# Optimization experiments

Measured on AMD Instinct MI355X. Metric: run time of the kernel, lower is better.

## Reference

```python
import jax, jax.numpy as jnp
import numpy as np

M = 1024       # input feature dim
T_EXPERTS = 64 # number of experts
K = 2          # top-k
TOKENS = 65536 # B*N flattened tokens


def setup_inputs() -> dict:
    key = jax.random.key(0)
    ks = jax.random.split(key, 6)
    return {
        "x": jax.random.normal(ks[0], (TOKENS, M), dtype=jnp.float32),
        "noise": jax.random.normal(ks[1], (TOKENS, T_EXPERTS), dtype=jnp.float32),
        "Wg_w": jax.random.normal(ks[2], (T_EXPERTS, M), dtype=jnp.float32) * 0.02,
        "Wg_b": jax.random.normal(ks[3], (T_EXPERTS,), dtype=jnp.float32) * 0.02,
        "Wn_w": jax.random.normal(ks[4], (T_EXPERTS, M), dtype=jnp.float32) * 0.02,
        "Wn_b": jax.random.normal(ks[5], (T_EXPERTS,), dtype=jnp.float32) * 0.02,
    }


def reference(x, noise, Wg_w, Wg_b, Wn_w, Wn_b):
    # logits = Wg(x); noise_scale = softplus(Wnoise(x))
    logits = jnp.einsum("bm,tm->bt", x, Wg_w) + Wg_b          # [tokens, t]
    noise_scale = jax.nn.softplus(jnp.einsum("bm,tm->bt", x, Wn_w) + Wn_b)
    H = logits + noise * noise_scale                           # noisy logits
    topk_vals, topk_idx = jax.lax.top_k(H, K)                  # [tokens, k]
    topk_softmax = jax.nn.softmax(topk_vals, axis=-1)
    # scatter softmax weights into sparse [tokens, t] gate tensor
    rows = jnp.arange(H.shape[0])[:, None]
    gates = jnp.zeros_like(H).at[rows, topk_idx].set(topk_softmax)
    return (gates, H, topk_idx, noise_scale, logits)
```

## Files before the change

kernel.cpp:

```cpp
#include <hip/hip_runtime.h>
#include <math.h>

#define NTOK 65536
#define MDIM 1024
#define NE   64
#define TB   128
#define NKC  32
#define DELTA 5e-4f

typedef float f32x4  __attribute__((ext_vector_type(4)));
typedef float f32x2  __attribute__((ext_vector_type(2)));
typedef short bf16x8 __attribute__((ext_vector_type(8)));
typedef unsigned int u32;

__device__ __forceinline__ unsigned short f32_to_bf16_rne(float f) {
    u32 u = __builtin_bit_cast(u32, f);
    u32 r = u + 0x7FFFu + ((u >> 16) & 1u);
    return (unsigned short)(r >> 16);
}
__device__ __forceinline__ float bf16_to_f32(unsigned short h) {
    u32 u = ((u32)h) << 16;
    return __builtin_bit_cast(float, u);
}
__device__ __forceinline__ void gll16(const void* g, void* l) {
    __builtin_amdgcn_global_load_lds(
        (const __attribute__((address_space(1))) u32*)g,
        (__attribute__((address_space(3))) u32*)l, 16, 0, 0);
}
__device__ __forceinline__ void nt_store4(float* p, f32x4 v) {
    __builtin_nontemporal_store(v, (f32x4*)p);
}

__global__ __launch_bounds__(256) void split_w_kernel(
    const float* __restrict__ Wg_w, const float* __restrict__ Wn_w,
    unsigned short* __restrict__ ws, u32* __restrict__ cnt)
{
    if (blockIdx.x == 0 && threadIdx.x == 0) *cnt = 0;

    const int gid  = blockIdx.x * 256 + threadIdx.x;
    const int kc   = gid >> 10;
    const int rest = gid & 1023;
    const int tm   = rest >> 8;
    const int mat  = (rest >> 7) & 1;
    const int sp   = (rest >> 6) & 1;
    const int lane = rest & 63;
    const int e    = (lane & 15) + 16 * tm;
    const int k0   = kc * 32 + 8 * (lane >> 4);
    const float* W = mat ? Wn_w : Wg_w;

    unsigned short o[8];
#pragma unroll
    for (int i = 0; i < 8; ++i) {
        const float v = W[(size_t)e * MDIM + k0 + i];
        const u32 u  = __builtin_bit_cast(u32, v);
        const unsigned short hb = (unsigned short)(u >> 16);
        o[i] = sp ? f32_to_bf16_rne(v - bf16_to_f32(hb)) : hb;
    }
    uint4 pk;
    pk.x = (u32)o[0] | ((u32)o[1] << 16);
    pk.y = (u32)o[2] | ((u32)o[3] << 16);
    pk.z = (u32)o[4] | ((u32)o[5] << 16);
    pk.w = (u32)o[6] | ((u32)o[7] << 16);
    *reinterpret_cast<uint4*>(&ws[(size_t)gid * 8]) = pk;
}

__global__ __launch_bounds__(512, 6) void gate_mfma_kernel(
    const float* __restrict__ x,
    const float* __restrict__ noise,
    const unsigned short* __restrict__ ws,
    const float* __restrict__ Wg_b,
    const float* __restrict__ Wn_b,
    float* __restrict__ out_gates,
    float* __restrict__ out_H,
    float* __restrict__ out_idx,
    float* __restrict__ out_ns,
    float* __restrict__ out_logits,
    u32* __restrict__ cnt,
    u32* __restrict__ list)
{
    __shared__ unsigned short wbuf[2][8192];

    const int tid   = threadIdx.x;
    const int lane  = tid & 63;
    const int w     = tid >> 6;
    const int c     = lane & 15;
    const int q     = lane >> 4;
    const int tokw  = blockIdx.x * TB + w * 16;
    const int phase = blockIdx.x & (NKC - 1);

    const float* __restrict__ xr = x + (size_t)(tokw + c) * MDIM + 8 * q;

    f32x4 acc[4][2];
#pragma unroll
    for (int tm = 0; tm < 4; ++tm)
#pragma unroll
        for (int m = 0; m < 2; ++m)
            acc[tm][m] = (f32x4){0.f, 0.f, 0.f, 0.f};

    f32x4 xa, xb;

#define STAGE(CI, BUF)                                                          \
    {                                                                           \
        const unsigned short* wc_ = ws + (size_t)(CI) * 8192;                   \
        gll16(wc_ + (size_t)tid * 8,         &wbuf[BUF][(size_t)tid * 8]);      \
        gll16(wc_ + (size_t)(tid + 512) * 8, &wbuf[BUF][(size_t)(tid + 512) * 8]); \
        __builtin_amdgcn_sched_barrier(0);                                      \
        xa = *reinterpret_cast<const f32x4*>(xr + (CI) * 32);                   \
        xb = *reinterpret_cast<const f32x4*>(xr + (CI) * 32 + 4);               \
        __builtin_amdgcn_sched_barrier(0);                                      \
    }

    STAGE(phase, 0)
    asm volatile("s_waitcnt vmcnt(2)" ::: "memory");
    __syncthreads();

    int cur = 0;
    for (int kci = 0; kci < NKC; ++kci) {
        asm volatile("s_waitcnt vmcnt(0)" ::: "memory");

        bf16x8 xhi, xlo;
        {
            const float v[8] = {xa.x, xa.y, xa.z, xa.w, xb.x, xb.y, xb.z, xb.w};
            u32 hp[4], lp[4];
#pragma unroll
            for (int p = 0; p < 4; ++p) {
                const u32 u0 = __builtin_bit_cast(u32, v[2 * p]);
                const u32 u1 = __builtin_bit_cast(u32, v[2 * p + 1]);
                const float h0 = __builtin_bit_cast(float, u0 & 0xFFFF0000u);
                const float h1 = __builtin_bit_cast(float, u1 & 0xFFFF0000u);
                hp[p] = (u0 >> 16) | (u1 & 0xFFFF0000u);
                const u32 l0 = (u32)f32_to_bf16_rne(v[2 * p] - h0);
                const u32 l1 = (u32)f32_to_bf16_rne(v[2 * p + 1] - h1);
                lp[p] = l0 | (l1 << 16);
            }
            const uint4 h4 = {hp[0], hp[1], hp[2], hp[3]};
            const uint4 l4 = {lp[0], lp[1], lp[2], lp[3]};
            xhi = __builtin_bit_cast(bf16x8, h4);
            xlo = __builtin_bit_cast(bf16x8, l4);
        }

        if (kci + 1 < NKC) {
            const int kcn = (kci + 1 + phase) & (NKC - 1);
            STAGE(kcn, cur ^ 1)
        }

#pragma unroll
        for (int tm = 0; tm < 4; ++tm)
#pragma unroll
            for (int mat = 0; mat < 2; ++mat) {
                const int gbase = ((tm * 4 + mat * 2) * 64 + lane) * 8;
                const bf16x8 whi = *reinterpret_cast<const bf16x8*>(&wbuf[cur][gbase]);
                const bf16x8 wlo = *reinterpret_cast<const bf16x8*>(&wbuf[cur][gbase + 512]);
                f32x4 a = acc[tm][mat];
                a = __builtin_amdgcn_mfma_f32_16x16x32_bf16(wlo, xhi, a, 0, 0, 0);
                a = __builtin_amdgcn_mfma_f32_16x16x32_bf16(whi, xlo, a, 0, 0, 0);
                a = __builtin_amdgcn_mfma_f32_16x16x32_bf16(whi, xhi, a, 0, 0, 0);
                acc[tm][mat] = a;
            }

        if (kci + 1 < NKC) {
            asm volatile("s_waitcnt vmcnt(2)" ::: "memory");
            __syncthreads();
        }
        cur ^= 1;
    }
#undef STAGE

    f32x4 bgv[4], bnv[4];
#pragma unroll
    for (int tm = 0; tm < 4; ++tm) {
        bgv[tm] = *reinterpret_cast<const f32x4*>(&Wg_b[16 * tm + 4 * q]);
        bnv[tm] = *reinterpret_cast<const f32x4*>(&Wn_b[16 * tm + 4 * q]);
    }

    const int tok = tokw + c;
    float hv[4][4];

#pragma unroll
    for (int tm = 0; tm < 4; ++tm) {
        const size_t rb = (size_t)tok * NE + 16 * tm + 4 * q;
        const f32x4 nz = __builtin_nontemporal_load(
            reinterpret_cast<const f32x4*>(&noise[rb]));
        f32x4 lg, nsv, hh;
#pragma unroll
        for (int r = 0; r < 4; ++r) {
            lg[r] = acc[tm][0][r] + bgv[tm][r];
            const float nl = acc[tm][1][r] + bnv[tm][r];
            nsv[r] = fmaxf(nl, 0.f) + log1pf(expf(-fabsf(nl)));
            hh[r]  = fmaf(nz[r], nsv[r], lg[r]);
            hv[tm][r] = hh[r];
        }
        nt_store4(&out_logits[rb], lg);
        nt_store4(&out_ns[rb],     nsv);
        nt_store4(&out_H[rb],      hh);
    }

    float v1 = -INFINITY, v2 = -INFINITY, v3 = -INFINITY;
    int   i1 = 0,         i2 = 0;
#pragma unroll
    for (int tm = 0; tm < 4; ++tm)
#pragma unroll
        for (int r = 0; r < 4; ++r) {
            const int ex = 16 * tm + 4 * q + r;
            const float hcur = hv[tm][r];
            if (hcur > v1)      { v3 = v2; v2 = v1; i2 = i1; v1 = hcur; i1 = ex; }
            else if (hcur > v2) { v3 = v2; v2 = hcur; i2 = ex; }
            else if (hcur > v3) { v3 = hcur; }
        }

#pragma unroll
    for (int off = 16; off <= 32; off <<= 1) {
        const float w1 = __shfl_xor(v1, off, 64);
        const int   k1 = __shfl_xor(i1, off, 64);
        const float w2 = __shfl_xor(v2, off, 64);
        const int   k2 = __shfl_xor(i2, off, 64);
        const float w3 = __shfl_xor(v3, off, 64);
        float m3;
        if (v1 >= w1) m3 = (v2 >= w1) ? fmaxf(v3, w1) : fmaxf(v2, w2);
        else          m3 = (w2 >= v1) ? fmaxf(w3, v1) : fmaxf(w2, v2);
        if (w1 > v1 || (w1 == v1 && k1 < i1)) {
            if (v1 > w2 || (v1 == w2 && i1 < k2)) { v2 = v1; i2 = i1; }
            else                                  { v2 = w2; i2 = k2; }
            v1 = w1; i1 = k1;
        } else {
            if (w1 > v2 || (w1 == v2 && k1 < i2)) { v2 = w1; i2 = k1; }
        }
        v3 = m3;
    }

    const float e2v = expf(v2 - v1);
    const float inv = 1.f / (1.f + e2v);
    const float p1  = inv;
    const float p2  = e2v * inv;

#pragma unroll
    for (int tm = 0; tm < 4; ++tm) {
        f32x4 g;
#pragma unroll
        for (int r = 0; r < 4; ++r) {
            const int ex = 16 * tm + 4 * q + r;
            g[r] = (ex == i1) ? p1 : ((ex == i2) ? p2 : 0.f);
        }
        nt_store4(&out_gates[(size_t)tok * NE + 16 * tm + 4 * q], g);
    }
    if (q == 0) {
        f32x2 iv;
        iv.x = (float)i1;
        iv.y = (float)i2;
        __builtin_nontemporal_store(iv,
            reinterpret_cast<f32x2*>(&out_idx[(size_t)tok * 2]));
        if ((v1 - v2 < DELTA) || (v2 - v3 < DELTA)) {
            const u32 slot = atomicAdd(cnt, 1u);
            list[slot] = (u32)tok;
        }
    }
}

__global__ __launch_bounds__(64) void refine_kernel(
    const float* __restrict__ x,
    const float* __restrict__ noise,
    const float* __restrict__ Wg_w, const float* __restrict__ Wg_b,
    const float* __restrict__ Wn_w, const float* __restrict__ Wn_b,
    const u32* __restrict__ cnt, const u32* __restrict__ list,
    float* __restrict__ out_gates, float* __restrict__ out_idx)
{
    const int lane = threadIdx.x;
    const u32 n = *cnt;

    for (u32 it = blockIdx.x; it < n; it += gridDim.x) {
        const int tok = (int)list[it];

        f32x4 xv[4];
#pragma unroll
        for (int i = 0; i < 4; ++i)
            xv[i] = *reinterpret_cast<const f32x4*>(
                &x[(size_t)tok * MDIM + lane * 16 + i * 4]);

        float lgv = 0.f, nlv = 0.f;
        for (int e = 0; e < NE; ++e) {
            float sg = 0.f, sn = 0.f;
#pragma unroll
            for (int i = 0; i < 4; ++i) {
                const f32x4 wg = *reinterpret_cast<const f32x4*>(
                    &Wg_w[(size_t)e * MDIM + lane * 16 + i * 4]);
                const f32x4 wn = *reinterpret_cast<const f32x4*>(
                    &Wn_w[(size_t)e * MDIM + lane * 16 + i * 4]);
#pragma unroll
                for (int j = 0; j < 4; ++j) {
                    sg = fmaf(xv[i][j], wg[j], sg);
                    sn = fmaf(xv[i][j], wn[j], sn);
                }
            }
#pragma unroll
            for (int off = 32; off >= 1; off >>= 1) {
                sg += __shfl_xor(sg, off, 64);
                sn += __shfl_xor(sn, off, 64);
            }
            if (e == lane) { lgv = sg; nlv = sn; }
        }

        lgv += Wg_b[lane];
        nlv += Wn_b[lane];
        const float ns = fmaxf(nlv, 0.f) + log1pf(expf(-fabsf(nlv)));
        const float h  = fmaf(noise[(size_t)tok * NE + lane], ns, lgv);

        float v1 = h; int i1 = lane;
#pragma unroll
        for (int off = 32; off >= 1; off >>= 1) {
            const float ov = __shfl_xor(v1, off, 64);
            const int   oi = __shfl_xor(i1, off, 64);
            if (ov > v1 || (ov == v1 && oi < i1)) { v1 = ov; i1 = oi; }
        }
        float v2 = (lane == i1) ? -INFINITY : h; int i2 = lane;
#pragma unroll
        for (int off = 32; off >= 1; off >>= 1) {
            const float ov = __shfl_xor(v2, off, 64);
            const int   oi = __shfl_xor(i2, off, 64);
            if (ov > v2 || (ov == v2 && oi < i2)) { v2 = ov; i2 = oi; }
        }

        const float e2v = expf(v2 - v1);
        const float inv = 1.f / (1.f + e2v);
        const float p1  = inv;
        const float p2  = e2v * inv;

        out_gates[(size_t)tok * NE + lane] =
            (lane == i1) ? p1 : ((lane == i2) ? p2 : 0.f);
        if (lane == 0) {
            *reinterpret_cast<float2*>(&out_idx[(size_t)tok * 2]) =
                make_float2((float)i1, (float)i2);
        }
    }
}

extern "C" void kernel_launch(void* const* d_in, const int* in_sizes, int n_in,
                              void* d_out, int out_size, void* d_ws, size_t ws_size,
                              hipStream_t stream) {
    const float* x     = (const float*)d_in[0];
    const float* noise = (const float*)d_in[1];
    const float* Wg_w  = (const float*)d_in[2];
    const float* Wg_b  = (const float*)d_in[3];
    const float* Wn_w  = (const float*)d_in[4];
    const float* Wn_b  = (const float*)d_in[5];

    float* out = (float*)d_out;
    float* out_gates  = out;
    float* out_H      = out + (size_t)NTOK * NE;
    float* out_idx    = out + (size_t)2 * NTOK * NE;
    float* out_ns     = out + (size_t)2 * NTOK * NE + (size_t)NTOK * 2;
    float* out_logits = out + (size_t)3 * NTOK * NE + (size_t)NTOK * 2;

    unsigned short* wsplit = (unsigned short*)d_ws;
    u32* cnt  = (u32*)((char*)d_ws + 524288);
    u32* list = (u32*)((char*)d_ws + 524304);

    split_w_kernel<<<dim3(128), dim3(256), 0, stream>>>(Wg_w, Wn_w, wsplit, cnt);
    gate_mfma_kernel<<<dim3(NTOK / TB), dim3(512), 0, stream>>>(
        x, noise, wsplit, Wg_b, Wn_b,
        out_gates, out_H, out_idx, out_ns, out_logits, cnt, list);
    refine_kernel<<<dim3(1024), dim3(64), 0, stream>>>(
        x, noise, Wg_w, Wg_b, Wn_w, Wn_b, cnt, list, out_gates, out_idx);
}
```

Baseline: 121.0 us.

## Prefetch x fragments two k-chunks ahead with double-buffered registers

The x register loads are split from the weight LDS staging and issued two iterations ahead into a pair of register sets. The top-of-loop full vmcnt(0) wait goes away and the end-of-iteration waits are adjusted, so global x loads have more time in flight. Launch bounds drop from 6 to 5 waves per SIMD so the extra registers fit, which may lower occupancy.

```diff
diff --git a/kernel.cpp b/kernel.cpp
--- a/kernel.cpp
+++ b/kernel.cpp
@@ -64,7 +64,7 @@
     *reinterpret_cast<uint4*>(&ws[(size_t)gid * 8]) = pk;
 }
 
-__global__ __launch_bounds__(512, 6) void gate_mfma_kernel(
+__global__ __launch_bounds__(512, 5) void gate_mfma_kernel(
     const float* __restrict__ x,
     const float* __restrict__ noise,
     const unsigned short* __restrict__ ws,
@@ -97,30 +97,37 @@
         for (int m = 0; m < 2; ++m)
             acc[tm][m] = (f32x4){0.f, 0.f, 0.f, 0.f};
 
-    f32x4 xa, xb;
-
-#define STAGE(CI, BUF)                                                          \
+    f32x4 xa[2], xb[2];
+
+#define WGLL(CI, BUF)                                                           \
     {                                                                           \
         const unsigned short* wc_ = ws + (size_t)(CI) * 8192;                   \
         gll16(wc_ + (size_t)tid * 8,         &wbuf[BUF][(size_t)tid * 8]);      \
         gll16(wc_ + (size_t)(tid + 512) * 8, &wbuf[BUF][(size_t)(tid + 512) * 8]); \
         __builtin_amdgcn_sched_barrier(0);                                      \
-        xa = *reinterpret_cast<const f32x4*>(xr + (CI) * 32);                   \
-        xb = *reinterpret_cast<const f32x4*>(xr + (CI) * 32 + 4);               \
+    }
+#define XLOAD(CI, SET)                                                          \
+    {                                                                           \
+        xa[SET] = *reinterpret_cast<const f32x4*>(xr + (CI) * 32);              \
+        xb[SET] = *reinterpret_cast<const f32x4*>(xr + (CI) * 32 + 4);          \
         __builtin_amdgcn_sched_barrier(0);                                      \
     }
 
-    STAGE(phase, 0)
+    WGLL(phase, 0)
+    XLOAD(phase, 0)
+    XLOAD((phase + 1) & (NKC - 1), 1)
     asm volatile("s_waitcnt vmcnt(2)" ::: "memory");
     __syncthreads();
 
     int cur = 0;
     for (int kci = 0; kci < NKC; ++kci) {
-        asm volatile("s_waitcnt vmcnt(0)" ::: "memory");
+        const int st = kci & 1;
 
         bf16x8 xhi, xlo;
         {
-            const float v[8] = {xa.x, xa.y, xa.z, xa.w, xb.x, xb.y, xb.z, xb.w};
+            const f32x4 a = xa[st];
+            const f32x4 b = xb[st];
+            const float v[8] = {a.x, a.y, a.z, a.w, b.x, b.y, b.z, b.w};
             u32 hp[4], lp[4];
 #pragma unroll
             for (int p = 0; p < 4; ++p) {
@@ -138,10 +145,13 @@
             xhi = __builtin_bit_cast(bf16x8, h4);
             xlo = __builtin_bit_cast(bf16x8, l4);
         }
+        __builtin_amdgcn_sched_barrier(0);
 
         if (kci + 1 < NKC) {
-            const int kcn = (kci + 1 + phase) & (NKC - 1);
-            STAGE(kcn, cur ^ 1)
+            WGLL((kci + 1 + phase) & (NKC - 1), cur ^ 1)
+        }
+        if (kci + 2 < NKC) {
+            XLOAD((kci + 2 + phase) & (NKC - 1), st)
         }
 
 #pragma unroll
@@ -159,12 +169,17 @@
             }
 
         if (kci + 1 < NKC) {
-            asm volatile("s_waitcnt vmcnt(2)" ::: "memory");
+            if (kci + 2 < NKC) {
+                asm volatile("s_waitcnt vmcnt(2)" ::: "memory");
+            } else {
+                asm volatile("s_waitcnt vmcnt(0)" ::: "memory");
+            }
             __syncthreads();
         }
         cur ^= 1;
     }
-#undef STAGE
+#undef WGLL
+#undef XLOAD
 
     f32x4 bgv[4], bnv[4];
 #pragma unroll
```

Result: slower. 145.0 us (+19.8%).
